# Optimization experiments

Measured on AMD Instinct MI355X. Metric: run time of the kernel, lower is better.

Reference implementation:

```python
import jax, jax.numpy as jnp
import numpy as np

NEG_SLOPE = 0.2  # PyG GATConv default negative_slope
BN_EPS = 1e-5


def _segment_softmax(logits, seg, num_segments):
    # numerically stable softmax over edges grouped by destination node
    m = jax.ops.segment_max(logits, seg, num_segments=num_segments)
    e = jnp.exp(logits - m[seg])
    s = jax.ops.segment_sum(e, seg, num_segments=num_segments)
    return e / s[seg]


def _gat_conv(x, src, dst, W, a_src, a_dst, bias, heads, d_head, concat):
    N = x.shape[0]
    h = (x @ W).reshape(N, heads, d_head)                      # [N, H, D]
    alpha_src = jnp.einsum('nhd,hd->nh', h, a_src)             # [N, H]
    alpha_dst = jnp.einsum('nhd,hd->nh', h, a_dst)             # [N, H]
    logits = jax.nn.leaky_relu(alpha_src[src] + alpha_dst[dst], NEG_SLOPE)  # [E, H]
    alpha = _segment_softmax(logits, dst, N)                   # [E, H]
    msg = h[src] * alpha[:, :, None]                           # [E, H, D]
    out = jax.ops.segment_sum(msg, dst, num_segments=N)        # [N, H, D]
    out = out.reshape(N, heads * d_head) if concat else out.mean(axis=1)
    return out + bias


def setup_inputs() -> dict:
    key = jax.random.key(0)
    ks = jax.random.split(key, 12)
    N, E = 50000, 800000
    in_dim, hidden, out_dim, heads = 256, 128, 2, 4
    d1 = hidden // heads  # 32
    s = 0.05
    return {
        'x': jax.random.normal(ks[0], (N, in_dim), dtype=jnp.float32),
        'edge_index': jax.random.randint(ks[1], (2, E), 0, N, dtype=jnp.int64),
        'W1': jax.random.normal(ks[2], (in_dim, heads * d1), dtype=jnp.float32) * s,
        'att_src1': jax.random.normal(ks[3], (heads, d1), dtype=jnp.float32) * s,
        'att_dst1': jax.random.normal(ks[4], (heads, d1), dtype=jnp.float32) * s,
        'b1': jnp.zeros((heads * d1,), dtype=jnp.float32),
        'bn_gamma': jnp.ones((hidden,), dtype=jnp.float32),
        'bn_beta': jnp.zeros((hidden,), dtype=jnp.float32),
        'bn_mean': jnp.zeros((hidden,), dtype=jnp.float32),
        'bn_var': jnp.ones((hidden,), dtype=jnp.float32),
        'W2': jax.random.normal(ks[5], (hidden, out_dim), dtype=jnp.float32) * s,
        'att_src2': jax.random.normal(ks[6], (1, out_dim), dtype=jnp.float32) * s,
        'att_dst2': jax.random.normal(ks[7], (1, out_dim), dtype=jnp.float32) * s,
        'b2': jnp.zeros((out_dim,), dtype=jnp.float32),
    }


def reference(x, edge_index, W1, att_src1, att_dst1, b1,
              bn_gamma, bn_beta, bn_mean, bn_var,
              W2, att_src2, att_dst2, b2):
    N = x.shape[0]
    # PyG GATConv adds self-loops by default
    loop = jnp.arange(N, dtype=edge_index.dtype)
    src = jnp.concatenate([edge_index[0], loop])
    dst = jnp.concatenate([edge_index[1], loop])

    heads, d1 = att_src1.shape
    h = _gat_conv(x, src, dst, W1, att_src1, att_dst1, b1, heads, d1, concat=True)
    # BatchNorm1d in eval mode (running stats), then ReLU (dropout is a no-op in eval)
    h = (h - bn_mean) * jax.lax.rsqrt(bn_var + BN_EPS) * bn_gamma + bn_beta
    h = jax.nn.relu(h)
    out = _gat_conv(h, src, dst, W2, att_src2, att_dst2, b2, 1, att_src2.shape[1], concat=False)
    return out
```

## Files before the change

kernel.cpp:

```cpp
#include <hip/hip_runtime.h>
#include <hip/hip_bf16.h>

#define LRELU(x) ((x) > 0.f ? (x) : 0.2f * (x))
#define CAP 96
#define BINBITS 7
#define BINCAP 2600
#define WSTR 104

typedef short bf16x8 __attribute__((ext_vector_type(8)));
typedef float f32x4 __attribute__((ext_vector_type(4)));

__device__ __forceinline__ float b2f(unsigned short u) {
  union { unsigned int i; float f; } v;
  v.i = ((unsigned int)u) << 16;
  return v.f;
}
__device__ __forceinline__ unsigned short f2b(float f) {
  unsigned int u = __float_as_uint(f);
  unsigned int r = (u + 0x7fffu + ((u >> 16) & 1u)) >> 16;
  return (unsigned short)r;
}

__device__ __forceinline__ void acc2(float w, unsigned int p, float& a0,
                                     float& a1) {
  union { unsigned int u; float f; } lo, hi;
  lo.u = p << 16;
  hi.u = p & 0xffff0000u;
  a0 = fmaf(w, lo.f, a0);
  a1 = fmaf(w, hi.f, a1);
}

__global__ __launch_bounds__(256) void setup_kernel(
    const float* __restrict__ W, unsigned short* __restrict__ w1t,
    int* __restrict__ gcnt) {
  const int tid = threadIdx.x;
  if (blockIdx.x == 0) {
    gcnt[tid] = 0;
    gcnt[256 + tid] = 0;
  }
  int idx = blockIdx.x * 256 + tid;
  int n = idx >> 8, k = idx & 255;
  w1t[idx] = f2b(W[k * 128 + n]);
}

__global__ __launch_bounds__(512) void gemm1_mfma_kernel(
    const float* __restrict__ x, const unsigned short* __restrict__ w1t,
    const float* __restrict__ atts, const float* __restrict__ attd,
    unsigned short* __restrict__ h1bf, float* __restrict__ asrc,
    float* __restrict__ adst, int N) {
  __shared__ unsigned short bsh[128 * 264];

  const int tid = threadIdx.x;
  const int m0 = blockIdx.x * 128 + (tid >> 6) * 16;
  const bool active = (m0 < N);
  const int lane = tid & 63;
  const int row = lane & 15;
  const int quad = lane >> 4;

  const float* ap = x + (size_t)(m0 + row) * 256 + quad * 8;
  f32x4 xa[8], xb[8];
  if (active) {
#pragma unroll
    for (int k = 0; k < 8; k++) {
      xa[k] = *(const f32x4*)(ap + k * 32);
      xb[k] = *(const f32x4*)(ap + k * 32 + 4);
    }
  }
  __builtin_amdgcn_sched_barrier(0);

#pragma unroll
  for (int i = 0; i < 8; i++) {
    int idx = (i * 512 + tid) * 8;
    int brow = idx >> 8;
    int k = idx & 255;
    *(uint4*)(bsh + brow * 264 + k) = *(const uint4*)(w1t + brow * 256 + k);
  }
  __syncthreads();
  if (!active) return;

  f32x4 acc[8];
#pragma unroll
  for (int t = 0; t < 8; t++) acc[t] = (f32x4){0.f, 0.f, 0.f, 0.f};

#pragma unroll
  for (int ks = 0; ks < 8; ks++) {
    const float af[8] = {xa[ks][0], xa[ks][1], xa[ks][2], xa[ks][3],
                         xb[ks][0], xb[ks][1], xb[ks][2], xb[ks][3]};
    bf16x8 ahi, alo;
#pragma unroll
    for (int j = 0; j < 8; j++) {
      unsigned short hh = f2b(af[j]);
      ahi[j] = (short)hh;
      alo[j] = (short)f2b(af[j] - b2f(hh));
    }
#pragma unroll
    for (int t = 0; t < 8; t++) {
      bf16x8 b = *(const bf16x8*)(bsh + (t * 16 + row) * 264 + ks * 32 + quad * 8);
      acc[t] = __builtin_amdgcn_mfma_f32_16x16x32_bf16(ahi, b, acc[t], 0, 0, 0);
      acc[t] = __builtin_amdgcn_mfma_f32_16x16x32_bf16(alo, b, acc[t], 0, 0, 0);
    }
  }

  unsigned short* op = h1bf + (size_t)(m0 + quad * 4) * 128 + row;
#pragma unroll
  for (int t = 0; t < 8; t++)
#pragma unroll
    for (int r = 0; r < 4; r++)
      op[(size_t)r * 128 + t * 16] = f2b(acc[t][r]);

  float asv[8], adv[8];
#pragma unroll
  for (int t = 0; t < 8; t++) {
    asv[t] = atts[t * 16 + row];
    adv[t] = attd[t * 16 + row];
  }
  float ps[4][4], pd[4][4];
#pragma unroll
  for (int h = 0; h < 4; h++)
#pragma unroll
    for (int r = 0; r < 4; r++) {
      ps[h][r] = acc[2 * h][r] * asv[2 * h] + acc[2 * h + 1][r] * asv[2 * h + 1];
      pd[h][r] = acc[2 * h][r] * adv[2 * h] + acc[2 * h + 1][r] * adv[2 * h + 1];
    }
#pragma unroll
  for (int o = 1; o < 16; o <<= 1) {
#pragma unroll
    for (int h = 0; h < 4; h++)
#pragma unroll
      for (int r = 0; r < 4; r++) {
        ps[h][r] += __shfl_xor(ps[h][r], o);
        pd[h][r] += __shfl_xor(pd[h][r], o);
      }
  }
  if (row == 0) {
#pragma unroll
    for (int r = 0; r < 4; r++) {
      int m = m0 + quad * 4 + r;
#pragma unroll
      for (int h = 0; h < 4; h++) {
        asrc[m * 4 + h] = ps[h][r];
        adst[m * 4 + h] = pd[h][r];
      }
    }
  }
}

__global__ __launch_bounds__(256) void bin_edges_kernel(
    const int* __restrict__ ei, int E, int* __restrict__ gcnt,
    unsigned int* __restrict__ binned, int nbins) {
  __shared__ int hist[512];
  __shared__ int base[512];
  const int tid = threadIdx.x;
  for (int i = tid; i < 512; i += 256) hist[i] = 0;
  __syncthreads();
  const int chunk = (E + gridDim.x - 1) / gridDim.x;
  const int e0 = blockIdx.x * chunk;
  const int e1 = min(e0 + chunk, E);
  for (int e = e0 + tid; e < e1; e += 256)
    atomicAdd(&hist[ei[(size_t)E + e] >> BINBITS], 1);
  __syncthreads();
  for (int i = tid; i < nbins; i += 256)
    if (hist[i] > 0) base[i] = atomicAdd(&gcnt[i], hist[i]);
  __syncthreads();
  for (int i = tid; i < 512; i += 256) hist[i] = 0;
  __syncthreads();
  for (int e = e0 + tid; e < e1; e += 256) {
    int s = ei[e];
    int t = ei[(size_t)E + e];
    int b = t >> BINBITS;
    int pos = base[b] + atomicAdd(&hist[b], 1);
    if (pos < BINCAP)
      binned[(size_t)b * BINCAP + pos] = ((unsigned int)t << 16) | (unsigned int)s;
  }
}

__global__ __launch_bounds__(256) void bin_to_buckets_kernel(
    const int* __restrict__ gcnt, const unsigned int* __restrict__ binned,
    int* __restrict__ cnt, unsigned short* __restrict__ buckets, int N) {
  __shared__ unsigned short lbkt[128 * CAP];
  __shared__ int lcnt[128];
  const int b = blockIdx.x;
  const int tid = threadIdx.x;
  if (tid < 128) lcnt[tid] = 0;
  __syncthreads();
  const int ne = min(gcnt[b], BINCAP);
  const unsigned int* bp = binned + (size_t)b * BINCAP;
  for (int i = tid; i < ne; i += 256) {
    unsigned int p = bp[i];
    int ln = (p >> 16) & 127;
    int pos = atomicAdd(&lcnt[ln], 1);
    if (pos < CAP) lbkt[ln * CAP + pos] = (unsigned short)(p & 0xffff);
  }
  __syncthreads();
  const int n0 = b << BINBITS;
  const int nn = min(128, N - n0);
  if (nn <= 0) return;
  if (tid < nn) cnt[n0 + tid] = lcnt[tid];
  const int total8 = (nn * CAP) >> 3;
  uint4* d4 = (uint4*)(buckets + (size_t)n0 * CAP);
  const uint4* s4 = (const uint4*)lbkt;
  for (int i = tid; i < total8; i += 256) d4[i] = s4[i];
}

__global__ __launch_bounds__(256) void agg1_kernel(
    const int* __restrict__ cnt, const unsigned short* __restrict__ buckets,
    const unsigned short* __restrict__ h1bf, const float* __restrict__ asrc,
    const float* __restrict__ adst, const float* __restrict__ b1,
    const float* __restrict__ gamma, const float* __restrict__ beta,
    const float* __restrict__ mean, const float* __restrict__ var,
    const float* __restrict__ W2, const float* __restrict__ as2,
    const float* __restrict__ ad2, float4* __restrict__ pk, int N) {
  __shared__ float wsh[4][4][WSTR];
  const int wv = __builtin_amdgcn_readfirstlane(threadIdx.x >> 6);
  const int t = blockIdx.x * 4 + wv;
  if (t >= N) return;
  const int l = threadIdx.x & 63;
  const int h = l >> 4;
  const int js = l & 15;
  const int c0 = 2 * l;
  const int nmax = N - 1;

  const unsigned short* bkt = buckets + (size_t)t * CAP;
  const int deg = min(__builtin_amdgcn_readfirstlane(cnt[t]), CAP);

  const float ad = adst[t * 4 + h];
  const float aself = asrc[t * 4 + h];
  const int sw0 = min((int)bkt[js], nmax);
  const float av0 = asrc[sw0 * 4 + h];
  float av1 = 0.f;
  if (deg > 16) {
    const int sw1 = min((int)bkt[16 + js], nmax);
    av1 = asrc[sw1 * 4 + h];
  }

  unsigned int p[32];
#define EXTR2(word, i)                                              \
  {                                                                 \
    unsigned int u_ = __builtin_amdgcn_readfirstlane(word);         \
    sa[i] = min((int)(u_ & 0xffffu), nmax);                         \
    sa[i + 1] = min((int)(u_ >> 16), nmax);                         \
  }
#define LOAD8(vec, base)                                            \
  {                                                                 \
    int sa[8];                                                      \
    EXTR2((vec).x, 0)                                               \
    EXTR2((vec).y, 2)                                               \
    EXTR2((vec).z, 4)                                               \
    EXTR2((vec).w, 6)                                               \
    _Pragma("unroll") for (int i_ = 0; i_ < 8; i_++) p[(base) + i_] = \
        *(const unsigned int*)(h1bf + (size_t)sa[i_] * 128 + c0);   \
  }
  if (deg > 0) { const uint4 v = *(const uint4*)(bkt);      LOAD8(v, 0) }
  if (deg > 8) { const uint4 v = *(const uint4*)(bkt + 8);  LOAD8(v, 8) }
  if (deg > 16) { const uint4 v = *(const uint4*)(bkt + 16); LOAD8(v, 16) }
  if (deg > 24) { const uint4 v = *(const uint4*)(bkt + 24); LOAD8(v, 24) }

  const float2 b1v = *(const float2*)(b1 + c0);
  const float2 mv = *(const float2*)(mean + c0);
  const float2 vv = *(const float2*)(var + c0);
  const float2 gv = *(const float2*)(gamma + c0);
  const float2 bb = *(const float2*)(beta + c0);
  const float4 w2v = *(const float4*)(W2 + c0 * 2);
  const float as20 = as2[0], as21 = as2[1];
  const float ad20 = ad2[0], ad21 = ad2[1];

  float* wrow = &wsh[wv][h][0];
  float w0 = (js < deg) ? __expf(LRELU(av0 + ad)) : 0.f;
  float w1 = (16 + js < deg) ? __expf(LRELU(av1 + ad)) : 0.f;
  wrow[js] = w0;
  wrow[16 + js] = w1;
  float denp = w0 + w1;
#pragma unroll
  for (int b = 2; b < 6; b++) {
    if (deg > (b << 4)) {
      const int idx = (b << 4) + js;
      const int s = min((int)bkt[idx], nmax);
      float w = (idx < deg) ? __expf(LRELU(asrc[s * 4 + h] + ad)) : 0.f;
      wrow[idx] = w;
      denp += w;
    }
  }
#pragma unroll
  for (int o = 1; o < 16; o <<= 1) denp += __shfl_xor(denp, o);
  const float wself = __expf(LRELU(aself + ad));
  const float den = denp + wself;

  float acc0 = 0.f, acc1 = 0.f;
#define ACC8(base)                                                  \
  {                                                                 \
    const f32x4 wa = *(const f32x4*)(wrow + (base));                \
    const f32x4 wb = *(const f32x4*)(wrow + (base) + 4);            \
    acc2(wa[0], p[(base) + 0], acc0, acc1);                         \
    acc2(wa[1], p[(base) + 1], acc0, acc1);                         \
    acc2(wa[2], p[(base) + 2], acc0, acc1);                         \
    acc2(wa[3], p[(base) + 3], acc0, acc1);                         \
    acc2(wb[0], p[(base) + 4], acc0, acc1);                         \
    acc2(wb[1], p[(base) + 5], acc0, acc1);                         \
    acc2(wb[2], p[(base) + 6], acc0, acc1);                         \
    acc2(wb[3], p[(base) + 7], acc0, acc1);                         \
  }
  if (deg > 0) ACC8(0)
  if (deg > 8) ACC8(8)
  if (deg > 16) ACC8(16)
  if (deg > 24) ACC8(24)
#pragma unroll
  for (int b = 2; b < 6; b++) {
    if (deg > (b << 4)) {
      const uint4 va = *(const uint4*)(bkt + (b << 4));
      const uint4 vb = *(const uint4*)(bkt + (b << 4) + 8);
      LOAD8(va, 0)
      LOAD8(vb, 8)
      const int base = b << 4;
      const f32x4 wa = *(const f32x4*)(wrow + base);
      const f32x4 wb2 = *(const f32x4*)(wrow + base + 4);
      const f32x4 wc = *(const f32x4*)(wrow + base + 8);
      const f32x4 wd = *(const f32x4*)(wrow + base + 12);
#pragma unroll
      for (int k = 0; k < 4; k++) acc2(wa[k], p[k], acc0, acc1);
#pragma unroll
      for (int k = 0; k < 4; k++) acc2(wb2[k], p[4 + k], acc0, acc1);
#pragma unroll
      for (int k = 0; k < 4; k++) acc2(wc[k], p[8 + k], acc0, acc1);
#pragma unroll
      for (int k = 0; k < 4; k++) acc2(wd[k], p[12 + k], acc0, acc1);
    }
  }
  {
    const unsigned int p0 = *(const unsigned int*)(h1bf + (size_t)t * 128 + c0);
    acc2(wself, p0, acc0, acc1);
  }
#undef EXTR2
#undef LOAD8
#undef ACC8

  const float sc0 = rsqrtf(vv.x + 1e-5f) * gv.x;
  const float sc1 = rsqrtf(vv.y + 1e-5f) * gv.y;
  const float of0 = (b1v.x - mv.x) * sc0 + bb.x;
  const float of1 = (b1v.y - mv.y) * sc1 + bb.y;
  const float inv = 1.f / den;
  float v0 = fmaf(acc0 * inv, sc0, of0);
  float v1 = fmaf(acc1 * inv, sc1, of1);
  v0 = v0 > 0.f ? v0 : 0.f;
  v1 = v1 > 0.f ? v1 : 0.f;

  float g0 = v0 * w2v.x + v1 * w2v.z;
  float g1 = v0 * w2v.y + v1 * w2v.w;
#pragma unroll
  for (int o = 32; o > 0; o >>= 1) {
    g0 += __shfl_down(g0, o);
    g1 += __shfl_down(g1, o);
  }
  if (l == 0) {
    float4 p4;
    p4.x = g0;
    p4.y = g1;
    p4.z = g0 * as20 + g1 * as21;
    p4.w = g0 * ad20 + g1 * ad21;
    pk[t] = p4;
  }
}

__global__ __launch_bounds__(256) void agg2_kernel(
    const int* __restrict__ cnt, const unsigned short* __restrict__ buckets,
    const float4* __restrict__ pk, const float* __restrict__ b2,
    float* __restrict__ out, int N) {
  const int t = blockIdx.x * 16 + (threadIdx.x >> 4);
  if (t >= N) return;
  const int lg = threadIdx.x & 15;
  float4 pt = pk[t];
  const float ad = pt.w;
  float a0 = 0.f, a1 = 0.f, den = 0.f;
  const unsigned short* bkt = buckets + (size_t)t * CAP;
  const int deg = min(cnt[t], CAP);
  for (int j = lg; j < deg; j += 16) {
    float4 p = pk[bkt[j]];
    float w = __expf(LRELU(p.z + ad));
    a0 += w * p.x;
    a1 += w * p.y;
    den += w;
  }
#pragma unroll
  for (int o = 8; o > 0; o >>= 1) {
    a0 += __shfl_xor(a0, o);
    a1 += __shfl_xor(a1, o);
    den += __shfl_xor(den, o);
  }
  if (lg == 0) {
    float w = __expf(LRELU(pt.z + ad));
    a0 += w * pt.x;
    a1 += w * pt.y;
    den += w;
    float2 o2;
    o2.x = a0 / den + b2[0];
    o2.y = a1 / den + b2[1];
    *(float2*)(out + (size_t)t * 2) = o2;
  }
}

extern "C" void kernel_launch(void* const* d_in, const int* in_sizes, int n_in,
                              void* d_out, int out_size, void* d_ws,
                              size_t ws_size, hipStream_t stream) {
  const float* x      = (const float*)d_in[0];
  const int*   ei     = (const int*)d_in[1];
  const float* W1     = (const float*)d_in[2];
  const float* atts1  = (const float*)d_in[3];
  const float* attd1  = (const float*)d_in[4];
  const float* b1     = (const float*)d_in[5];
  const float* gamma  = (const float*)d_in[6];
  const float* beta   = (const float*)d_in[7];
  const float* mean   = (const float*)d_in[8];
  const float* var    = (const float*)d_in[9];
  const float* W2     = (const float*)d_in[10];
  const float* atts2  = (const float*)d_in[11];
  const float* attd2  = (const float*)d_in[12];
  const float* b2     = (const float*)d_in[13];
  float* out = (float*)d_out;

  const int N = in_sizes[0] / 256;
  const int E = in_sizes[1] / 2;
  const int nbins = (N + (1 << BINBITS) - 1) >> BINBITS;

  char* ws = (char*)d_ws;
  size_t off = 0;
  unsigned short* h1bf = (unsigned short*)(ws + off); off += (size_t)N * 128 * 2;
  float* asrc1 = (float*)(ws + off); off += (size_t)N * 4 * 4;
  float* adst1 = (float*)(ws + off); off += (size_t)N * 4 * 4;
  float4* pk   = (float4*)(ws + off); off += (size_t)N * 16;
  int*   cnt   = (int*)  (ws + off); off += (size_t)N * 4;
  int*   gcnt  = (int*)  (ws + off); off += 512 * 4;
  unsigned short* w1t = (unsigned short*)(ws + off); off += 128 * 256 * 2;
  unsigned short* buckets = (unsigned short*)(ws + off);
  off += (size_t)N * CAP * 2;
  unsigned int* binned = (unsigned int*)(ws + off);
  off += (size_t)nbins * BINCAP * 4;

  setup_kernel<<<128, 256, 0, stream>>>(W1, w1t, gcnt);
  gemm1_mfma_kernel<<<(N + 127) / 128, 512, 0, stream>>>(
      x, w1t, atts1, attd1, h1bf, asrc1, adst1, N);
  bin_edges_kernel<<<512, 256, 0, stream>>>(ei, E, gcnt, binned, nbins);
  bin_to_buckets_kernel<<<nbins, 256, 0, stream>>>(gcnt, binned, cnt, buckets,
                                                   N);
  agg1_kernel<<<(N + 3) / 4, 256, 0, stream>>>(cnt, buckets, h1bf, asrc1,
                                               adst1, b1, gamma, beta, mean,
                                               var, W2, atts2, attd2, pk, N);
  agg2_kernel<<<(N + 15) / 16, 256, 0, stream>>>(cnt, buckets, pk, b2, out, N);
}
```

Before: 194.7 us.

## Fuse edge binning into GEMM launch as interleaved block roles

Merges the first-layer MFMA GEMM and the edge-binning pass into one launch. Even and odd block indices take different roles so binning blocks run alongside GEMM blocks, and both share one LDS buffer. This removes a kernel launch boundary and lets the memory-bound binning overlap the compute-heavy GEMM. In exchange, binning blocks carry the GEMM kernel's 512-thread, large-LDS footprint, which can lower occupancy, and the grid-size formula assumes at least 256 GEMM tiles.

```diff
diff --git a/kernel.cpp b/kernel.cpp
--- a/kernel.cpp
+++ b/kernel.cpp
@@ -43,15 +43,56 @@
   w1t[idx] = f2b(W[k * 128 + n]);
 }
 
-__global__ __launch_bounds__(512) void gemm1_mfma_kernel(
+__global__ __launch_bounds__(512) void gemm_bin_kernel(
     const float* __restrict__ x, const unsigned short* __restrict__ w1t,
     const float* __restrict__ atts, const float* __restrict__ attd,
     unsigned short* __restrict__ h1bf, float* __restrict__ asrc,
-    float* __restrict__ adst, int N) {
-  __shared__ unsigned short bsh[128 * 264];
-
+    float* __restrict__ adst, const int* __restrict__ ei, int E,
+    int* __restrict__ gcnt, unsigned int* __restrict__ binned, int nbins,
+    int N) {
+  __shared__ unsigned short smem[128 * 264];
+
+  const int bid = blockIdx.x;
   const int tid = threadIdx.x;
-  const int m0 = blockIdx.x * 128 + (tid >> 6) * 16;
+  int role_bin, widx;
+  if (bid < 512) {
+    role_bin = bid & 1;
+    widx = bid >> 1;
+  } else {
+    role_bin = 0;
+    widx = 256 + (bid - 512);
+  }
+
+  if (role_bin) {
+    int* hist = (int*)smem;
+    int* base = ((int*)smem) + 512;
+    hist[tid] = 0;
+    __syncthreads();
+    const int chunk = (E + 255) / 256;
+    const int e0 = widx * chunk;
+    const int e1 = min(e0 + chunk, E);
+    for (int e = e0 + tid; e < e1; e += 512)
+      atomicAdd(&hist[ei[(size_t)E + e] >> BINBITS], 1);
+    __syncthreads();
+    if (tid < nbins && hist[tid] > 0)
+      base[tid] = atomicAdd(&gcnt[tid], hist[tid]);
+    __syncthreads();
+    hist[tid] = 0;
+    __syncthreads();
+    for (int e = e0 + tid; e < e1; e += 512) {
+      int s = ei[e];
+      int t = ei[(size_t)E + e];
+      int b = t >> BINBITS;
+      int pos = base[b] + atomicAdd(&hist[b], 1);
+      if (pos < BINCAP)
+        binned[(size_t)b * BINCAP + pos] =
+            ((unsigned int)t << 16) | (unsigned int)s;
+    }
+    return;
+  }
+
+  unsigned short* bsh = smem;
+  const int m0 = widx * 128 + (tid >> 6) * 16;
   const bool active = (m0 < N);
   const int lane = tid & 63;
   const int row = lane & 15;
@@ -95,7 +136,8 @@
     }
 #pragma unroll
     for (int t = 0; t < 8; t++) {
-      bf16x8 b = *(const bf16x8*)(bsh + (t * 16 + row) * 264 + ks * 32 + quad * 8);
+      bf16x8 b =
+          *(const bf16x8*)(bsh + (t * 16 + row) * 264 + ks * 32 + quad * 8);
       acc[t] = __builtin_amdgcn_mfma_f32_16x16x32_bf16(ahi, b, acc[t], 0, 0, 0);
       acc[t] = __builtin_amdgcn_mfma_f32_16x16x32_bf16(alo, b, acc[t], 0, 0, 0);
     }
@@ -142,35 +184,6 @@
         adst[m * 4 + h] = pd[h][r];
       }
     }
-  }
-}
-
-__global__ __launch_bounds__(256) void bin_edges_kernel(
-    const int* __restrict__ ei, int E, int* __restrict__ gcnt,
-    unsigned int* __restrict__ binned, int nbins) {
-  __shared__ int hist[512];
-  __shared__ int base[512];
-  const int tid = threadIdx.x;
-  for (int i = tid; i < 512; i += 256) hist[i] = 0;
-  __syncthreads();
-  const int chunk = (E + gridDim.x - 1) / gridDim.x;
-  const int e0 = blockIdx.x * chunk;
-  const int e1 = min(e0 + chunk, E);
-  for (int e = e0 + tid; e < e1; e += 256)
-    atomicAdd(&hist[ei[(size_t)E + e] >> BINBITS], 1);
-  __syncthreads();
-  for (int i = tid; i < nbins; i += 256)
-    if (hist[i] > 0) base[i] = atomicAdd(&gcnt[i], hist[i]);
-  __syncthreads();
-  for (int i = tid; i < 512; i += 256) hist[i] = 0;
-  __syncthreads();
-  for (int e = e0 + tid; e < e1; e += 256) {
-    int s = ei[e];
-    int t = ei[(size_t)E + e];
-    int b = t >> BINBITS;
-    int pos = base[b] + atomicAdd(&hist[b], 1);
-    if (pos < BINCAP)
-      binned[(size_t)b * BINCAP + pos] = ((unsigned int)t << 16) | (unsigned int)s;
   }
 }
 
@@ -434,10 +447,10 @@
   unsigned int* binned = (unsigned int*)(ws + off);
   off += (size_t)nbins * BINCAP * 4;
 
+  const int ngemm = (N + 127) / 128;
   setup_kernel<<<128, 256, 0, stream>>>(W1, w1t, gcnt);
-  gemm1_mfma_kernel<<<(N + 127) / 128, 512, 0, stream>>>(
-      x, w1t, atts1, attd1, h1bf, asrc1, adst1, N);
-  bin_edges_kernel<<<512, 256, 0, stream>>>(ei, E, gcnt, binned, nbins);
+  gemm_bin_kernel<<<512 + (ngemm - 256), 512, 0, stream>>>(
+      x, w1t, atts1, attd1, h1bf, asrc1, adst1, ei, E, gcnt, binned, nbins, N);
   bin_to_buckets_kernel<<<nbins, 256, 0, stream>>>(gcnt, binned, cnt, buckets,
                                                    N);
   agg1_kernel<<<(N + 3) / 4, 256, 0, stream>>>(cnt, buckets, h1bf, asrc1,
```

Result: faster. 184.0 us (-5.5%).
